# Performance work log

Measured on AMD Instinct MI355X. Metric: run time of the kernel, lower is better.

## Reference

```python
import jax, jax.numpy as jnp
import numpy as np

FORGET_BIAS = 1.0  # tf.nn.rnn_cell.LSTMCell default
HIDDEN = 64


def setup_inputs() -> dict:
    key = jax.random.key(0)
    k1, k2 = jax.random.split(key)
    B, T, D = 4096, 9, 512
    x = jax.random.normal(k1, (B, T, D), dtype=jnp.float32)
    # Fused LSTM kernel: [(D + H), 4H], gate order (i, j, f, o) as in TF LSTMCell
    kernel = jax.random.normal(k2, (D + HIDDEN, 4 * HIDDEN), dtype=jnp.float32) * 0.02
    bias = jnp.zeros((4 * HIDDEN,), dtype=jnp.float32)
    return {"x": x, "kernel": kernel, "bias": bias}


def _lstm_scan(x, kernel, bias):
    B, T, D = x.shape
    H = HIDDEN
    # Split kernel into input and recurrent parts for a cleaner scan body.
    Wx = kernel[:D]          # [D, 4H]
    Wh = kernel[D:]          # [H, 4H]
    # Precompute input contributions for all timesteps in one big GEMM.
    xg = jnp.einsum('btd,dg->btg', x, Wx) + bias  # [B, T, 4H]

    def step(carry, xg_t):
        c, h = carry
        gates = xg_t + h @ Wh  # [B, 4H]
        i, j, f, o = jnp.split(gates, 4, axis=-1)  # TF gate order: i, j, f, o
        c_new = jax.nn.sigmoid(f + FORGET_BIAS) * c + jax.nn.sigmoid(i) * jnp.tanh(j)
        h_new = jax.nn.sigmoid(o) * jnp.tanh(c_new)
        return (c_new, h_new), h_new

    c0 = jnp.zeros((B, H), dtype=x.dtype)
    h0 = jnp.zeros((B, H), dtype=x.dtype)
    _, hs = jax.lax.scan(step, (c0, h0), jnp.swapaxes(xg, 0, 1))  # hs: [T, B, H]
    return jnp.transpose(hs, (1, 0, 2))  # [B, T, H]


def reference(x, kernel, bias):
    return _lstm_scan(x, kernel, bias)
```

## Files before the change

kernel.cpp:

```cpp
#include <hip/hip_runtime.h>
#include <math.h>

#define T_STEPS 9
#define D_IN    512
#define HID     64
#define G4      256
#define BPB     16
#define MT      144
#define UPAD    84

typedef short  short8 __attribute__((ext_vector_type(8)));
typedef float  f32x4  __attribute__((ext_vector_type(4)));
typedef unsigned int uint;
typedef unsigned short ushort;

__device__ __forceinline__ ushort f2bf(float f) {
    uint u = __float_as_uint(f);
    u = (u + 0x7FFFu + ((u >> 16) & 1u)) >> 16;
    return (ushort)u;
}
__device__ __forceinline__ float bf2f(ushort b) {
    return __uint_as_float(((uint)b) << 16);
}
__device__ __forceinline__ float fsig(float x) {
    return 1.0f / (1.0f + __expf(-x));
}
__device__ __forceinline__ float ftanh(float x) {
    float t = __expf(-2.0f * fabsf(x));
    float r = (1.0f - t) / (1.0f + t);
    return copysignf(r, x);
}
__device__ __forceinline__ void gl_lds16(const void* g, void* l) {
    __builtin_amdgcn_global_load_lds(
        (const __attribute__((address_space(1))) unsigned int*)g,
        (__attribute__((address_space(3))) unsigned int*)l, 16, 0, 0);
}

__global__ __launch_bounds__(256)
void prep_w(const float* __restrict__ kern, ushort* __restrict__ wxT,
            ushort* __restrict__ whT)
{
    int i = blockIdx.x * 256 + threadIdx.x;
    if (i < 131072) {
        int j  = i & 7;
        int n  = (i >> 3) & 255;
        int qk = (i >> 11) & 3;
        int k0 = i >> 13;
        int k  = k0 * 32 + qk * 8 + j;
        wxT[i] = f2bf(kern[(size_t)k * G4 + n]);
    } else {
        int i2 = i - 131072;
        int j  = i2 & 7;
        int n  = (i2 >> 3) & 255;
        int kq = i2 >> 11;
        whT[i2] = f2bf(kern[(size_t)(D_IN + kq * 8 + j) * G4 + n]);
    }
}

__global__ __launch_bounds__(256, 1)
void lstm_fused(const float* __restrict__ x, const ushort* __restrict__ wxT,
                const ushort* __restrict__ whT, const float* __restrict__ bias,
                float* __restrict__ out)
{
    __shared__ ushort sXg[4 * MT * UPAD];
    __shared__ ushort sWh[8 * 256 * 8];
    __shared__ ushort sB [4 * 256 * 8];
    __shared__ ushort sA [4 * MT * 8];
    __shared__ ushort sH [8 * 16 * 8];

    const int t = threadIdx.x;
    const int w = t >> 6, l = t & 63;
    const int lane15 = l & 15, quad = l >> 4;
    const int u = w * 16 + lane15;

    {
        const char* g = (const char*)whT;
        char* s = (char*)sWh;
        #pragma unroll
        for (int q = 0; q < 8; ++q) {
            int off = (w * 8 + q) * 1024;
            gl_lds16(g + off + l * 16, s + off);
        }
    }

    const float* xblk = x + (size_t)blockIdx.x * MT * D_IN;
    const int m_a  = t >> 1, kh_a = t & 1;
    const int m_b  = 128 + (t >> 1);
    const float* pA = xblk + (size_t)m_a * D_IN + kh_a * 16;
    const float* pB = xblk + (size_t)m_b * D_IN + kh_a * 16;

    float4 rA[4], rB[4];
    #pragma unroll
    for (int q = 0; q < 4; ++q) rA[q] = ((const float4*)pA)[q];
    if (t < 32) {
        #pragma unroll
        for (int q = 0; q < 4; ++q) rB[q] = ((const float4*)pB)[q];
    }

    f32x4 acc[9][4];
    #pragma unroll
    for (int i = 0; i < 9; ++i)
        #pragma unroll
        for (int j = 0; j < 4; ++j)
            acc[i][j] = (f32x4){0.f, 0.f, 0.f, 0.f};

    for (int k0 = 0; k0 < 16; ++k0) {
        __syncthreads();
        {
            uint4 lo, hi;
            lo.x = f2bf(rA[0].x) | ((uint)f2bf(rA[0].y) << 16);
            lo.y = f2bf(rA[0].z) | ((uint)f2bf(rA[0].w) << 16);
            lo.z = f2bf(rA[1].x) | ((uint)f2bf(rA[1].y) << 16);
            lo.w = f2bf(rA[1].z) | ((uint)f2bf(rA[1].w) << 16);
            hi.x = f2bf(rA[2].x) | ((uint)f2bf(rA[2].y) << 16);
            hi.y = f2bf(rA[2].z) | ((uint)f2bf(rA[2].w) << 16);
            hi.z = f2bf(rA[3].x) | ((uint)f2bf(rA[3].y) << 16);
            hi.w = f2bf(rA[3].z) | ((uint)f2bf(rA[3].w) << 16);
            *(uint4*)&sA[((kh_a * 2 + 0) * MT + m_a) * 8] = lo;
            *(uint4*)&sA[((kh_a * 2 + 1) * MT + m_a) * 8] = hi;
            if (t < 32) {
                uint4 lo2, hi2;
                lo2.x = f2bf(rB[0].x) | ((uint)f2bf(rB[0].y) << 16);
                lo2.y = f2bf(rB[0].z) | ((uint)f2bf(rB[0].w) << 16);
                lo2.z = f2bf(rB[1].x) | ((uint)f2bf(rB[1].y) << 16);
                lo2.w = f2bf(rB[1].z) | ((uint)f2bf(rB[1].w) << 16);
                hi2.x = f2bf(rB[2].x) | ((uint)f2bf(rB[2].y) << 16);
                hi2.y = f2bf(rB[2].z) | ((uint)f2bf(rB[2].w) << 16);
                hi2.z = f2bf(rB[3].x) | ((uint)f2bf(rB[3].y) << 16);
                hi2.w = f2bf(rB[3].z) | ((uint)f2bf(rB[3].w) << 16);
                *(uint4*)&sA[((kh_a * 2 + 0) * MT + m_b) * 8] = lo2;
                *(uint4*)&sA[((kh_a * 2 + 1) * MT + m_b) * 8] = hi2;
            }
        }
        {
            const char* gb = (const char*)wxT + (size_t)k0 * 16384;
            char* lb = (char*)sB;
            #pragma unroll
            for (int q = 0; q < 4; ++q) {
                int off = w * 4096 + q * 1024;
                gl_lds16(gb + off + l * 16, lb + off);
            }
        }
        __syncthreads();

        if (k0 < 15) {
            const float4* nA = (const float4*)(pA + (k0 + 1) * 32);
            #pragma unroll
            for (int q = 0; q < 4; ++q) rA[q] = nA[q];
            if (t < 32) {
                const float4* nB = (const float4*)(pB + (k0 + 1) * 32);
                #pragma unroll
                for (int q = 0; q < 4; ++q) rB[q] = nB[q];
            }
        }

        short8 bF[4];
        #pragma unroll
        for (int j = 0; j < 4; ++j)
            bF[j] = *(const short8*)&sB[(quad * 256 + j * 64 + w * 16 + lane15) * 8];
        #pragma unroll
        for (int i = 0; i < 9; ++i) {
            short8 aF = *(const short8*)&sA[(quad * MT + i * 16 + lane15) * 8];
            #pragma unroll
            for (int j = 0; j < 4; ++j)
                acc[i][j] = __builtin_amdgcn_mfma_f32_16x16x32_bf16(aF, bF[j], acc[i][j], 0, 0, 0);
        }
    }

    #pragma unroll
    for (int i = 0; i < 9; ++i)
        #pragma unroll
        for (int j = 0; j < 4; ++j)
            #pragma unroll
            for (int r = 0; r < 4; ++r) {
                int m = i * 16 + quad * 4 + r;
                sXg[(j * MT + m) * UPAD + u] = f2bf(acc[i][j][r]);
            }

    ((uint2*)sH)[t] = (uint2){0u, 0u};

    float bia[4];
    bia[0] = bias[u];
    bia[1] = bias[64 + u];
    bia[2] = bias[128 + u] + 1.0f;
    bia[3] = bias[192 + u];

    float cst[4] = {0.f, 0.f, 0.f, 0.f};
    const int b0 = blockIdx.x * BPB;
    __syncthreads();

    for (int step = 0; step < T_STEPS; ++step) {
        f32x4 g4[4];
        #pragma unroll
        for (int g = 0; g < 4; ++g) {
            #pragma unroll
            for (int r = 0; r < 4; ++r) {
                int m = (quad * 4 + r) * T_STEPS + step;
                g4[g][r] = bf2f(sXg[(g * MT + m) * UPAD + u]) + bia[g];
            }
        }
        short8 aF[2];
        #pragma unroll
        for (int kh = 0; kh < 2; ++kh)
            aF[kh] = *(const short8*)&sH[((kh * 4 + quad) * 16 + lane15) * 8];
        #pragma unroll
        for (int g = 0; g < 4; ++g) {
            #pragma unroll
            for (int kh = 0; kh < 2; ++kh) {
                short8 bF = *(const short8*)&sWh[((kh * 4 + quad) * 256 + g * 64 + u) * 8];
                g4[g] = __builtin_amdgcn_mfma_f32_16x16x32_bf16(aF[kh], bF, g4[g], 0, 0, 0);
            }
        }
        __syncthreads();

        #pragma unroll
        for (int r = 0; r < 4; ++r) {
            int bi = quad * 4 + r;
            float ii = fsig(g4[0][r]);
            float jj = ftanh(g4[1][r]);
            float ff = fsig(g4[2][r]);
            float oo = fsig(g4[3][r]);
            float c = ff * cst[r] + ii * jj;
            cst[r] = c;
            float h = oo * ftanh(c);
            out[((size_t)(b0 + bi) * T_STEPS + step) * HID + u] = h;
            sH[((u >> 3) * 16 + bi) * 8 + (u & 7)] = f2bf(h);
        }
        __syncthreads();
    }
}

extern "C" void kernel_launch(void* const* d_in, const int* in_sizes, int n_in,
                              void* d_out, int out_size, void* d_ws, size_t ws_size,
                              hipStream_t stream)
{
    const float* x    = (const float*)d_in[0];
    const float* kern = (const float*)d_in[1];
    const float* bias = (const float*)d_in[2];
    float* out = (float*)d_out;

    const int B = in_sizes[0] / (T_STEPS * D_IN);

    ushort* wxT = (ushort*)d_ws;
    ushort* whT = (ushort*)((char*)d_ws + 262144);

    prep_w<<<576, 256, 0, stream>>>(kern, wxT, whT);
    lstm_fused<<<B / BPB, 256, 0, stream>>>(x, wxT, whT, bias, out);
}
```

Baseline: 136.4 us.

## Keep input-gate accumulators in registers and halve batch per block

Reorders the input GEMM rows as (step, batch) so each 16-row MFMA tile holds two timesteps of 8 batch rows. The recurrent loop can then read the precomputed gates straight from accumulator registers instead of a large shared-memory staging buffer. Wx and Wh fragments are now read directly from global memory into registers rather than staged in LDS, and the smaller LDS footprint allows two blocks per CU with twice as many blocks. The cost is that half the lanes sit idle in each recurrent step, cell state moves between lane halves via a shuffle, the A tile is padded to 80 rows with zero rows, and Wx is re-fetched from global or cache by every block.

```diff
diff --git a/kernel.cpp b/kernel.cpp
--- a/kernel.cpp
+++ b/kernel.cpp
@@ -5,9 +5,8 @@
 #define D_IN    512
 #define HID     64
 #define G4      256
-#define BPB     16
-#define MT      144
-#define UPAD    84
+#define BPB     8
+#define MTP     80
 
 typedef short  short8 __attribute__((ext_vector_type(8)));
 typedef float  f32x4  __attribute__((ext_vector_type(4)));
@@ -19,9 +18,6 @@
     u = (u + 0x7FFFu + ((u >> 16) & 1u)) >> 16;
     return (ushort)u;
 }
-__device__ __forceinline__ float bf2f(ushort b) {
-    return __uint_as_float(((uint)b) << 16);
-}
 __device__ __forceinline__ float fsig(float x) {
     return 1.0f / (1.0f + __expf(-x));
 }
@@ -29,11 +25,6 @@
     float t = __expf(-2.0f * fabsf(x));
     float r = (1.0f - t) / (1.0f + t);
     return copysignf(r, x);
-}
-__device__ __forceinline__ void gl_lds16(const void* g, void* l) {
-    __builtin_amdgcn_global_load_lds(
-        (const __attribute__((address_space(1))) unsigned int*)g,
-        (__attribute__((address_space(3))) unsigned int*)l, 16, 0, 0);
 }
 
 __global__ __launch_bounds__(256)
@@ -57,56 +48,51 @@
     }
 }
 
-__global__ __launch_bounds__(256, 1)
+__global__ __launch_bounds__(256, 2)
 void lstm_fused(const float* __restrict__ x, const ushort* __restrict__ wxT,
                 const ushort* __restrict__ whT, const float* __restrict__ bias,
                 float* __restrict__ out)
 {
-    __shared__ ushort sXg[4 * MT * UPAD];
-    __shared__ ushort sWh[8 * 256 * 8];
-    __shared__ ushort sB [4 * 256 * 8];
-    __shared__ ushort sA [4 * MT * 8];
-    __shared__ ushort sH [8 * 16 * 8];
+    __shared__ ushort sA[4 * MTP * 8];
+    __shared__ ushort sH[8 * 16 * 8];
 
     const int t = threadIdx.x;
     const int w = t >> 6, l = t & 63;
     const int lane15 = l & 15, quad = l >> 4;
     const int u = w * 16 + lane15;
 
-    {
-        const char* g = (const char*)whT;
-        char* s = (char*)sWh;
-        #pragma unroll
-        for (int q = 0; q < 8; ++q) {
-            int off = (w * 8 + q) * 1024;
-            gl_lds16(g + off + l * 16, s + off);
-        }
-    }
-
-    const float* xblk = x + (size_t)blockIdx.x * MT * D_IN;
-    const int m_a  = t >> 1, kh_a = t & 1;
-    const int m_b  = 128 + (t >> 1);
-    const float* pA = xblk + (size_t)m_a * D_IN + kh_a * 16;
-    const float* pB = xblk + (size_t)m_b * D_IN + kh_a * 16;
-
-    float4 rA[4], rB[4];
+    short8 whF[4][2];
     #pragma unroll
-    for (int q = 0; q < 4; ++q) rA[q] = ((const float4*)pA)[q];
-    if (t < 32) {
-        #pragma unroll
-        for (int q = 0; q < 4; ++q) rB[q] = ((const float4*)pB)[q];
-    }
-
-    f32x4 acc[9][4];
+    for (int g = 0; g < 4; ++g)
+        #pragma unroll
+        for (int kh = 0; kh < 2; ++kh)
+            whF[g][kh] = *(const short8*)&whT[(size_t)((kh * 4 + quad) * 256 + g * 64 + u) * 8];
+
+    ((uint2*)sH)[t] = (uint2){0u, 0u};
+
+    const float* xblk = x + (size_t)blockIdx.x * (BPB * T_STEPS) * D_IN;
+    const int mhalf = t >> 1, kh_a = t & 1;
+    const bool ld = (mhalf < BPB * T_STEPS);
+    const bool zr = (!ld && mhalf < MTP);
+    const int b_ = mhalf & 7, s_ = mhalf >> 3;
+    const float* pA = xblk + (size_t)(b_ * T_STEPS + s_) * D_IN + kh_a * 16;
+
+    float4 rA[4];
+    if (ld) {
+        #pragma unroll
+        for (int q = 0; q < 4; ++q) rA[q] = ((const float4*)pA)[q];
+    }
+
+    f32x4 acc[5][4];
     #pragma unroll
-    for (int i = 0; i < 9; ++i)
-        #pragma unroll
-        for (int j = 0; j < 4; ++j)
-            acc[i][j] = (f32x4){0.f, 0.f, 0.f, 0.f};
+    for (int i = 0; i < 5; ++i)
+        #pragma unroll
+        for (int g = 0; g < 4; ++g)
+            acc[i][g] = (f32x4){0.f, 0.f, 0.f, 0.f};
 
     for (int k0 = 0; k0 < 16; ++k0) {
         __syncthreads();
-        {
+        if (ld) {
             uint4 lo, hi;
             lo.x = f2bf(rA[0].x) | ((uint)f2bf(rA[0].y) << 16);
             lo.y = f2bf(rA[0].z) | ((uint)f2bf(rA[0].w) << 16);
@@ -116,68 +102,35 @@
             hi.y = f2bf(rA[2].z) | ((uint)f2bf(rA[2].w) << 16);
             hi.z = f2bf(rA[3].x) | ((uint)f2bf(rA[3].y) << 16);
             hi.w = f2bf(rA[3].z) | ((uint)f2bf(rA[3].w) << 16);
-            *(uint4*)&sA[((kh_a * 2 + 0) * MT + m_a) * 8] = lo;
-            *(uint4*)&sA[((kh_a * 2 + 1) * MT + m_a) * 8] = hi;
-            if (t < 32) {
-                uint4 lo2, hi2;
-                lo2.x = f2bf(rB[0].x) | ((uint)f2bf(rB[0].y) << 16);
-                lo2.y = f2bf(rB[0].z) | ((uint)f2bf(rB[0].w) << 16);
-                lo2.z = f2bf(rB[1].x) | ((uint)f2bf(rB[1].y) << 16);
-                lo2.w = f2bf(rB[1].z) | ((uint)f2bf(rB[1].w) << 16);
-                hi2.x = f2bf(rB[2].x) | ((uint)f2bf(rB[2].y) << 16);
-                hi2.y = f2bf(rB[2].z) | ((uint)f2bf(rB[2].w) << 16);
-                hi2.z = f2bf(rB[3].x) | ((uint)f2bf(rB[3].y) << 16);
-                hi2.w = f2bf(rB[3].z) | ((uint)f2bf(rB[3].w) << 16);
-                *(uint4*)&sA[((kh_a * 2 + 0) * MT + m_b) * 8] = lo2;
-                *(uint4*)&sA[((kh_a * 2 + 1) * MT + m_b) * 8] = hi2;
-            }
-        }
-        {
-            const char* gb = (const char*)wxT + (size_t)k0 * 16384;
-            char* lb = (char*)sB;
-            #pragma unroll
-            for (int q = 0; q < 4; ++q) {
-                int off = w * 4096 + q * 1024;
-                gl_lds16(gb + off + l * 16, lb + off);
-            }
-        }
-        __syncthreads();
-
-        if (k0 < 15) {
+            *(uint4*)&sA[((kh_a * 2 + 0) * MTP + mhalf) * 8] = lo;
+            *(uint4*)&sA[((kh_a * 2 + 1) * MTP + mhalf) * 8] = hi;
+        } else if (zr) {
+            uint4 z = {0u, 0u, 0u, 0u};
+            *(uint4*)&sA[((kh_a * 2 + 0) * MTP + mhalf) * 8] = z;
+            *(uint4*)&sA[((kh_a * 2 + 1) * MTP + mhalf) * 8] = z;
+        }
+        __syncthreads();
+
+        if (ld && k0 < 15) {
             const float4* nA = (const float4*)(pA + (k0 + 1) * 32);
             #pragma unroll
             for (int q = 0; q < 4; ++q) rA[q] = nA[q];
-            if (t < 32) {
-                const float4* nB = (const float4*)(pB + (k0 + 1) * 32);
-                #pragma unroll
-                for (int q = 0; q < 4; ++q) rB[q] = nB[q];
-            }
-        }
-
+        }
+
+        const ushort* wxc = wxT + (size_t)(k0 * 4 + quad) * 256 * 8;
         short8 bF[4];
         #pragma unroll
-        for (int j = 0; j < 4; ++j)
-            bF[j] = *(const short8*)&sB[(quad * 256 + j * 64 + w * 16 + lane15) * 8];
-        #pragma unroll
-        for (int i = 0; i < 9; ++i) {
-            short8 aF = *(const short8*)&sA[(quad * MT + i * 16 + lane15) * 8];
-            #pragma unroll
-            for (int j = 0; j < 4; ++j)
-                acc[i][j] = __builtin_amdgcn_mfma_f32_16x16x32_bf16(aF, bF[j], acc[i][j], 0, 0, 0);
-        }
-    }
-
-    #pragma unroll
-    for (int i = 0; i < 9; ++i)
-        #pragma unroll
-        for (int j = 0; j < 4; ++j)
-            #pragma unroll
-            for (int r = 0; r < 4; ++r) {
-                int m = i * 16 + quad * 4 + r;
-                sXg[(j * MT + m) * UPAD + u] = f2bf(acc[i][j][r]);
-            }
-
-    ((uint2*)sH)[t] = (uint2){0u, 0u};
+        for (int g = 0; g < 4; ++g)
+            bF[g] = *(const short8*)&wxc[(size_t)(g * 64 + u) * 8];
+
+        #pragma unroll
+        for (int i = 0; i < 5; ++i) {
+            short8 aF = *(const short8*)&sA[(quad * MTP + i * 16 + lane15) * 8];
+            #pragma unroll
+            for (int g = 0; g < 4; ++g)
+                acc[i][g] = __builtin_amdgcn_mfma_f32_16x16x32_bf16(aF, bF[g], acc[i][g], 0, 0, 0);
+        }
+    }
 
     float bia[4];
     bia[0] = bias[u];
@@ -187,44 +140,49 @@
 
     float cst[4] = {0.f, 0.f, 0.f, 0.f};
     const int b0 = blockIdx.x * BPB;
-    __syncthreads();
-
-    for (int step = 0; step < T_STEPS; ++step) {
+
+    for (int s = 0; s < T_STEPS; ++s) {
+        const int  i = s >> 1;
+        const int  p = s & 1;
+        const bool active = ((quad >> 1) == p);
+        const int  bofs = (quad & 1) * 4;
+
         f32x4 g4[4];
         #pragma unroll
-        for (int g = 0; g < 4; ++g) {
-            #pragma unroll
-            for (int r = 0; r < 4; ++r) {
-                int m = (quad * 4 + r) * T_STEPS + step;
-                g4[g][r] = bf2f(sXg[(g * MT + m) * UPAD + u]) + bia[g];
-            }
-        }
+        for (int g = 0; g < 4; ++g)
+            #pragma unroll
+            for (int r = 0; r < 4; ++r)
+                g4[g][r] = acc[i][g][r] + bia[g];
+
         short8 aF[2];
         #pragma unroll
         for (int kh = 0; kh < 2; ++kh)
             aF[kh] = *(const short8*)&sH[((kh * 4 + quad) * 16 + lane15) * 8];
-        #pragma unroll
-        for (int g = 0; g < 4; ++g) {
-            #pragma unroll
-            for (int kh = 0; kh < 2; ++kh) {
-                short8 bF = *(const short8*)&sWh[((kh * 4 + quad) * 256 + g * 64 + u) * 8];
-                g4[g] = __builtin_amdgcn_mfma_f32_16x16x32_bf16(aF[kh], bF, g4[g], 0, 0, 0);
+
+        #pragma unroll
+        for (int g = 0; g < 4; ++g)
+            #pragma unroll
+            for (int kh = 0; kh < 2; ++kh)
+                g4[g] = __builtin_amdgcn_mfma_f32_16x16x32_bf16(aF[kh], whF[g][kh], g4[g], 0, 0, 0);
+
+        __syncthreads();
+
+        const int wrow = 8 * ((s + 1) & 1);
+        #pragma unroll
+        for (int r = 0; r < 4; ++r) {
+            float cp = __shfl_xor(cst[r], 32);
+            if (active) {
+                float ii = fsig(g4[0][r]);
+                float jj = ftanh(g4[1][r]);
+                float ff = fsig(g4[2][r]);
+                float oo = fsig(g4[3][r]);
+                float c  = ff * cp + ii * jj;
+                cst[r] = c;
+                float h = oo * ftanh(c);
+                int bb = bofs + r;
+                out[((size_t)(b0 + bb) * T_STEPS + s) * HID + u] = h;
+                sH[((u >> 3) * 16 + wrow + bb) * 8 + (u & 7)] = f2bf(h);
             }
-        }
-        __syncthreads();
-
-        #pragma unroll
-        for (int r = 0; r < 4; ++r) {
-            int bi = quad * 4 + r;
-            float ii = fsig(g4[0][r]);
-            float jj = ftanh(g4[1][r]);
-            float ff = fsig(g4[2][r]);
-            float oo = fsig(g4[3][r]);
-            float c = ff * cst[r] + ii * jj;
-            cst[r] = c;
-            float h = oo * ftanh(c);
-            out[((size_t)(b0 + bi) * T_STEPS + step) * HID + u] = h;
-            sH[((u >> 3) * 16 + bi) * 8 + (u & 7)] = f2bf(h);
         }
         __syncthreads();
     }
```

After: 251.3 us. 84.3% more time.
